# Kernel tuning notes

Hardware: AMD Instinct MI355X
Metric: run time of the kernel (lower is better)

## Reference

```python
import jax, jax.numpy as jnp
import numpy as np

NR_AST_NODES = 500_000
NR_CFG_NODES = 100_000
NR_MAPPED = 400_000
AST_DIM = 256
CFG_DIM = 256


def setup_inputs() -> dict:
    key = jax.random.key(0)
    k1, k2, k3, k4, k5 = jax.random.split(key, 5)
    prev = jax.random.normal(k1, (NR_AST_NODES, AST_DIM), dtype=jnp.float32)
    cfg = jax.random.normal(k2, (NR_CFG_NODES, CFG_DIM), dtype=jnp.float32)
    # key indices: unique (a subset permutation) so the scatter is well-defined,
    # mirroring the one-update-per-AST-node mapping in the original data.
    map_key = jax.random.permutation(k3, NR_AST_NODES)[:NR_MAPPED].astype(jnp.int32)
    map_val = jax.random.randint(k4, (NR_MAPPED,), 0, NR_CFG_NODES, dtype=jnp.int32)
    kw1, kw2 = jax.random.split(k5)
    W_update = jax.random.normal(kw1, (CFG_DIM, AST_DIM), dtype=jnp.float32) / np.sqrt(CFG_DIM)
    b_update = jnp.zeros((AST_DIM,), dtype=jnp.float32)
    W_gate = jax.random.normal(kw2, (AST_DIM + AST_DIM, AST_DIM), dtype=jnp.float32) / np.sqrt(2 * AST_DIM)
    b_gate = jnp.zeros((AST_DIM,), dtype=jnp.float32)
    return {
        "previous_ast_nodes_encodings": prev,
        "new_cfg_nodes_encodings": cfg,
        "map_key_indices": map_key,
        "map_val_indices": map_val,
        "W_update": W_update,
        "b_update": b_update,
        "W_gate": W_gate,
        "b_gate": b_gate,
    }


def reference(previous_ast_nodes_encodings, new_cfg_nodes_encodings,
              map_key_indices, map_val_indices,
              W_update, b_update, W_gate, b_gate):
    # gather: previous AST-node states and the macro (CFG) context per mapping entry
    prev_g = previous_ast_nodes_encodings[map_key_indices]        # [M, ast_dim]
    ctx_g = new_cfg_nodes_encodings[map_val_indices]              # [M, cfg_dim]
    # gated StateUpdater (GRU-like gate):
    #   u = tanh(ctx @ W_update + b_update)            -- projected state update
    #   z = sigmoid([prev; u] @ W_gate + b_gate)       -- update gate
    #   new = z * prev + (1 - z) * u
    u = jnp.tanh(ctx_g @ W_update + b_update)                      # [M, ast_dim]
    z = jax.nn.sigmoid(
        prev_g @ W_gate[:AST_DIM] + u @ W_gate[AST_DIM:] + b_gate)  # [M, ast_dim]
    new_states = z * prev_g + (1.0 - z) * u                        # [M, ast_dim]
    # scatter updated rows back into the dense AST-node encodings (dim 0)
    return previous_ast_nodes_encodings.at[map_key_indices].set(new_states)
```

## Files before the change

kernel.cpp:

```cpp
#include <hip/hip_runtime.h>
#include <hip/hip_bf16.h>

#define AST_DIM 256
#define NR_AST 500000
#define NR_CFG 100000
#define NR_MAP 400000
#define NBLK_MAIN ((NR_AST + 63) / 64)

typedef short short8 __attribute__((ext_vector_type(8)));
typedef float f32x4 __attribute__((ext_vector_type(4)));
typedef unsigned long long u64;
typedef unsigned int u32;

__device__ __forceinline__ unsigned short f2bf(float f) {
    u32 u = __float_as_uint(f);
    u += 0x7FFFu + ((u >> 16) & 1u);
    return (unsigned short)(u >> 16);
}
__device__ __forceinline__ float bf2f(unsigned short s) {
    return __uint_as_float(((u32)s) << 16);
}
__device__ __forceinline__ u64 pack4(f32x4 v) {
    __hip_bfloat162 lo = __float22bfloat162_rn(float2{v.x, v.y});
    __hip_bfloat162 hi = __float22bfloat162_rn(float2{v.z, v.w});
    return (u64)(*(u32*)&lo) | ((u64)(*(u32*)&hi) << 32);
}
__device__ __forceinline__ float fast_tanh(float x) {
    return 1.f - 2.f * __builtin_amdgcn_rcpf(__expf(2.f * x) + 1.f);
}
__device__ __forceinline__ float fast_sigmoid(float x) {
    return __builtin_amdgcn_rcpf(1.f + __expf(-x));
}
__device__ __forceinline__ void dma16(const void* g, void* l) {
    __builtin_amdgcn_global_load_lds((const __attribute__((address_space(1))) u32*)g,
                                     (__attribute__((address_space(3))) u32*)l, 16, 0, 0);
}

__global__ void convert_w(const float* __restrict__ Wu, const float* __restrict__ Wg,
                          unsigned short* __restrict__ wt) {
    int idx = blockIdx.x * 256 + threadIdx.x;
    if (idx >= 3 * 65536) return;
    int m = idx >> 16;
    int r = idx & 65535;
    int n = r >> 8;
    int k = r & 255;
    float v;
    if (m == 0)      v = Wu[k * 256 + n];
    else if (m == 1) v = Wg[k * 256 + n];
    else             v = Wg[(k + 256) * 256 + n];
    wt[idx] = f2bf(v);
}

__global__ void build_vor(const int* __restrict__ keys, const int* __restrict__ vals,
                          int* __restrict__ vor) {
    int i = blockIdx.x * 256 + threadIdx.x;
    if (i < NR_MAP) vor[keys[i]] = vals[i];
}

__global__ __launch_bounds__(512, 4) void compute_u(
    const float* __restrict__ cfg, const unsigned short* __restrict__ Wtu,
    const float* __restrict__ bu, unsigned short* __restrict__ u_all) {
    __shared__ __align__(16) unsigned char ctxb[64 * 512];

    const int tid = threadIdx.x;
    const int lane = tid & 63;
    const int wv = tid >> 6;
    const int ln15 = lane & 15;
    const int khi = lane >> 4;
    const int cb = wv * 32;
    const int m0 = blockIdx.x * 64;

    f32x4 v[8];
#pragma unroll
    for (int i = 0; i < 8; ++i) {
        int g = m0 + wv * 8 + i;
        if (g >= NR_CFG) g = NR_CFG - 1;
        v[i] = *((const f32x4*)(cfg + (size_t)g * AST_DIM) + lane);
    }
    __builtin_amdgcn_sched_barrier(0);
#pragma unroll
    for (int i = 0; i < 8; ++i) {
        int r = wv * 8 + i;
        int addr = (r << 9) + ((lane << 3) ^ ((r & 7) << 4));
        *(u64*)(ctxb + addr) = pack4(v[i]);
    }
    __syncthreads();

    const float b0 = bu[cb + ln15], b1 = bu[cb + 16 + ln15];
    f32x4 acc[4][2];
#pragma unroll
    for (int mt = 0; mt < 4; ++mt) {
        acc[mt][0] = f32x4{b0, b0, b0, b0};
        acc[mt][1] = f32x4{b1, b1, b1, b1};
    }
#pragma unroll
    for (int ks = 0; ks < 8; ++ks) {
        short8 a[4], b[2];
#pragma unroll
        for (int mt = 0; mt < 4; ++mt) {
            int row = mt * 16 + ln15;
            int addr = (row << 9) + (((ks << 6) + (khi << 4)) ^ ((row & 7) << 4));
            a[mt] = *(const short8*)(ctxb + addr);
        }
#pragma unroll
        for (int nt = 0; nt < 2; ++nt)
            b[nt] = *(const short8*)(Wtu + (cb + nt * 16 + ln15) * 256 + ks * 32 + khi * 8);
#pragma unroll
        for (int mt = 0; mt < 4; ++mt)
#pragma unroll
            for (int nt = 0; nt < 2; ++nt)
                acc[mt][nt] = __builtin_amdgcn_mfma_f32_16x16x32_bf16(a[mt], b[nt], acc[mt][nt], 0, 0, 0);
    }
#pragma unroll
    for (int mt = 0; mt < 4; ++mt)
#pragma unroll
        for (int rr = 0; rr < 4; ++rr) {
            int row = mt * 16 + khi * 4 + rr;
            int g = m0 + row;
            if (g < NR_CFG) {
#pragma unroll
                for (int nt = 0; nt < 2; ++nt) {
                    int col = cb + nt * 16 + ln15;
                    u_all[(size_t)g * AST_DIM + col] = f2bf(fast_tanh(acc[mt][nt][rr]));
                }
            }
        }
}

__global__ __launch_bounds__(512, 4) void stream_main(
    const float* __restrict__ prev, const unsigned short* __restrict__ u_all,
    const int* __restrict__ vor,
    const unsigned short* __restrict__ Wtgt, const unsigned short* __restrict__ Wtgb,
    const float* __restrict__ bg, float* __restrict__ out) {
    __shared__ __align__(16) unsigned char prvb[64 * 512];
    __shared__ __align__(16) unsigned char u_st[64 * 512];

    const int tid = threadIdx.x;
    const int lane = tid & 63;
    const int wv = tid >> 6;
    const int ln15 = lane & 15;
    const int khi = lane >> 4;
    const int ln31 = lane & 31;
    const int cb = wv * 32;
    const int m0 = blockIdx.x * 64;

    int vr = -1;
    if (m0 + lane < NR_AST) vr = vor[m0 + lane];

    f32x4 v[8];
#pragma unroll
    for (int i = 0; i < 8; ++i) {
        int g = m0 + wv * 8 + i;
        if (g >= NR_AST) g = NR_AST - 1;
        v[i] = *((const f32x4*)(prev + (size_t)g * AST_DIM) + lane);
    }
    __builtin_amdgcn_sched_barrier(0);
#pragma unroll
    for (int i = 0; i < 4; ++i) {
        int r0 = wv * 8 + i * 2;
        int row = r0 + (lane >> 5);
        int vidx = __shfl(vr, row);
        int vsrc = vidx < 0 ? 0 : vidx;
        const unsigned short* src = u_all + (size_t)vsrc * AST_DIM + ((ln31 ^ (row & 7)) << 3);
        dma16(src, u_st + (r0 << 9));
    }
    __builtin_amdgcn_sched_barrier(0);
#pragma unroll
    for (int i = 0; i < 8; ++i) {
        int r = wv * 8 + i;
        int g = m0 + r;
        int addr = (r << 9) + ((lane << 3) ^ ((r & 7) << 4));
        *(u64*)(prvb + addr) = pack4(v[i]);
        if (g < NR_AST && __shfl(vr, r) < 0)
            *((f32x4*)(out + (size_t)g * AST_DIM) + lane) = v[i];
    }
    __syncthreads();

    const float b0 = bg[cb + ln15], b1 = bg[cb + 16 + ln15];
    f32x4 acc[4][2];
#pragma unroll
    for (int mt = 0; mt < 4; ++mt) {
        acc[mt][0] = f32x4{b0, b0, b0, b0};
        acc[mt][1] = f32x4{b1, b1, b1, b1};
    }
#pragma unroll
    for (int ks = 0; ks < 8; ++ks) {
        short8 a[4], bfr[2];
#pragma unroll
        for (int mt = 0; mt < 4; ++mt) {
            int row = mt * 16 + ln15;
            int addr = (row << 9) + (((ks << 6) + (khi << 4)) ^ ((row & 7) << 4));
            a[mt] = *(const short8*)(prvb + addr);
        }
#pragma unroll
        for (int nt = 0; nt < 2; ++nt)
            bfr[nt] = *(const short8*)(Wtgt + (cb + nt * 16 + ln15) * 256 + ks * 32 + khi * 8);
#pragma unroll
        for (int mt = 0; mt < 4; ++mt)
#pragma unroll
            for (int nt = 0; nt < 2; ++nt)
                acc[mt][nt] = __builtin_amdgcn_mfma_f32_16x16x32_bf16(a[mt], bfr[nt], acc[mt][nt], 0, 0, 0);
    }
#pragma unroll
    for (int ks = 0; ks < 8; ++ks) {
        short8 a[4], bfr[2];
#pragma unroll
        for (int mt = 0; mt < 4; ++mt) {
            int row = mt * 16 + ln15;
            int addr = (row << 9) + ((((ks << 2) + khi) ^ (row & 7)) << 4);
            a[mt] = *(const short8*)(u_st + addr);
        }
#pragma unroll
        for (int nt = 0; nt < 2; ++nt)
            bfr[nt] = *(const short8*)(Wtgb + (cb + nt * 16 + ln15) * 256 + ks * 32 + khi * 8);
#pragma unroll
        for (int mt = 0; mt < 4; ++mt)
#pragma unroll
            for (int nt = 0; nt < 2; ++nt)
                acc[mt][nt] = __builtin_amdgcn_mfma_f32_16x16x32_bf16(a[mt], bfr[nt], acc[mt][nt], 0, 0, 0);
    }

#pragma unroll
    for (int mt = 0; mt < 4; ++mt)
#pragma unroll
        for (int rr = 0; rr < 4; ++rr) {
            int row = mt * 16 + khi * 4 + rr;
            int g = m0 + row;
            int vrow = __shfl(vr, row);
            if (g < NR_AST && vrow >= 0) {
                float* orow = out + (size_t)g * AST_DIM;
#pragma unroll
                for (int nt = 0; nt < 2; ++nt) {
                    int col = cb + nt * 16 + ln15;
                    float z = fast_sigmoid(acc[mt][nt][rr]);
                    float pf = bf2f(*(const unsigned short*)(prvb + (row << 9) + ((col << 1) ^ ((row & 7) << 4))));
                    float uv = bf2f(*(const unsigned short*)(u_st + (row << 9) +
                                    ((((col >> 3) ^ (row & 7)) << 4) + ((col & 7) << 1))));
                    orow[col] = fmaf(z, pf - uv, uv);
                }
            }
        }
}

__global__ void set_mask(const int* __restrict__ keys, unsigned char* __restrict__ mask) {
    int i = blockIdx.x * 256 + threadIdx.x;
    if (i < NR_MAP) mask[keys[i]] = 1;
}

__global__ void copy_unmapped(const float* __restrict__ prev,
                              const unsigned char* __restrict__ mask,
                              float* __restrict__ out) {
    const long long total = (long long)NR_AST * 64;
    for (long long i = (long long)blockIdx.x * blockDim.x + threadIdx.x; i < total;
         i += (long long)gridDim.x * blockDim.x) {
        int row = (int)(i >> 6);
        if (!mask[row])
            ((f32x4*)out)[i] = ((const f32x4*)prev)[i];
    }
}

__global__ __launch_bounds__(512, 4) void mixer_fused(
    const float* __restrict__ prev, const float* __restrict__ cfg,
    const int* __restrict__ keys, const int* __restrict__ vals,
    const unsigned short* __restrict__ Wtu, const unsigned short* __restrict__ Wtgt,
    const unsigned short* __restrict__ Wtgb, const float* __restrict__ bu,
    const float* __restrict__ bg, float* __restrict__ out) {
    __shared__ __align__(16) unsigned char ctx_lds[64 * 512];
    __shared__ __align__(16) unsigned char prv_lds[64 * 512];

    const int tid = threadIdx.x;
    const int lane = tid & 63;
    const int wave = tid >> 6;
    const int ln15 = lane & 15;
    const int khi = lane >> 4;
    const int cb = wave * 32;
    const int m0 = blockIdx.x * 64;

    const int kv = keys[m0 + lane];
    const int vv = vals[m0 + lane];

#pragma unroll 4
    for (int i = 0; i < 8; ++i) {
        int r = i * 8 + wave;
        f32x4 cv = *((const f32x4*)(cfg + (size_t)__shfl(vv, r) * AST_DIM) + lane);
        f32x4 pv = *((const f32x4*)(prev + (size_t)__shfl(kv, r) * AST_DIM) + lane);
        int addr = (r << 9) + ((lane << 3) ^ ((r & 7) << 4));
        *(u64*)(ctx_lds + addr) = pack4(cv);
        *(u64*)(prv_lds + addr) = pack4(pv);
    }
    __syncthreads();

    f32x4 acc[4][2];
    {
        float b0 = bu[cb + ln15], b1 = bu[cb + 16 + ln15];
        for (int mt = 0; mt < 4; ++mt) {
            acc[mt][0] = f32x4{b0, b0, b0, b0};
            acc[mt][1] = f32x4{b1, b1, b1, b1};
        }
    }
#pragma unroll
    for (int ks = 0; ks < 8; ++ks) {
        short8 a[4], b[2];
        for (int mt = 0; mt < 4; ++mt) {
            int row = mt * 16 + ln15;
            int addr = (row << 9) + (((ks << 6) + (khi << 4)) ^ ((row & 7) << 4));
            a[mt] = *(const short8*)(ctx_lds + addr);
        }
        for (int nt = 0; nt < 2; ++nt)
            b[nt] = *(const short8*)(Wtu + (cb + nt * 16 + ln15) * 256 + ks * 32 + khi * 8);
        for (int mt = 0; mt < 4; ++mt)
            for (int nt = 0; nt < 2; ++nt)
                acc[mt][nt] = __builtin_amdgcn_mfma_f32_16x16x32_bf16(a[mt], b[nt], acc[mt][nt], 0, 0, 0);
    }
    __syncthreads();
#pragma unroll
    for (int mt = 0; mt < 4; ++mt)
        for (int rr = 0; rr < 4; ++rr) {
            int row = mt * 16 + khi * 4 + rr;
            for (int nt = 0; nt < 2; ++nt) {
                int col = cb + nt * 16 + ln15;
                int addr = (row << 9) + ((col << 1) ^ ((row & 7) << 4));
                *(unsigned short*)(ctx_lds + addr) = f2bf(fast_tanh(acc[mt][nt][rr]));
            }
        }
    __syncthreads();
    {
        float b0 = bg[cb + ln15], b1 = bg[cb + 16 + ln15];
        for (int mt = 0; mt < 4; ++mt) {
            acc[mt][0] = f32x4{b0, b0, b0, b0};
            acc[mt][1] = f32x4{b1, b1, b1, b1};
        }
    }
#pragma unroll
    for (int ks = 0; ks < 8; ++ks) {
        short8 a[4], b[2];
        for (int mt = 0; mt < 4; ++mt) {
            int row = mt * 16 + ln15;
            int addr = (row << 9) + (((ks << 6) + (khi << 4)) ^ ((row & 7) << 4));
            a[mt] = *(const short8*)(prv_lds + addr);
        }
        for (int nt = 0; nt < 2; ++nt)
            b[nt] = *(const short8*)(Wtgt + (cb + nt * 16 + ln15) * 256 + ks * 32 + khi * 8);
        for (int mt = 0; mt < 4; ++mt)
            for (int nt = 0; nt < 2; ++nt)
                acc[mt][nt] = __builtin_amdgcn_mfma_f32_16x16x32_bf16(a[mt], b[nt], acc[mt][nt], 0, 0, 0);
    }
#pragma unroll
    for (int ks = 0; ks < 8; ++ks) {
        short8 a[4], b[2];
        for (int mt = 0; mt < 4; ++mt) {
            int row = mt * 16 + ln15;
            int addr = (row << 9) + (((ks << 6) + (khi << 4)) ^ ((row & 7) << 4));
            a[mt] = *(const short8*)(ctx_lds + addr);
        }
        for (int nt = 0; nt < 2; ++nt)
            b[nt] = *(const short8*)(Wtgb + (cb + nt * 16 + ln15) * 256 + ks * 32 + khi * 8);
        for (int mt = 0; mt < 4; ++mt)
            for (int nt = 0; nt < 2; ++nt)
                acc[mt][nt] = __builtin_amdgcn_mfma_f32_16x16x32_bf16(a[mt], b[nt], acc[mt][nt], 0, 0, 0);
    }
#pragma unroll
    for (int mt = 0; mt < 4; ++mt)
        for (int rr = 0; rr < 4; ++rr) {
            int row = mt * 16 + khi * 4 + rr;
            int key = __shfl(kv, row);
            float* orow = out + (size_t)key * AST_DIM;
            for (int nt = 0; nt < 2; ++nt) {
                int col = cb + nt * 16 + ln15;
                int ad = (row << 9) + ((col << 1) ^ ((row & 7) << 4));
                float z = fast_sigmoid(acc[mt][nt][rr]);
                float pf = bf2f(*(const unsigned short*)(prv_lds + ad));
                float uv = bf2f(*(const unsigned short*)(ctx_lds + ad));
                orow[col] = fmaf(z, pf - uv, uv);
            }
        }
}

extern "C" void kernel_launch(void* const* d_in, const int* in_sizes, int n_in,
                              void* d_out, int out_size, void* d_ws, size_t ws_size,
                              hipStream_t stream) {
    const float* prev = (const float*)d_in[0];
    const float* cfg = (const float*)d_in[1];
    const int* keys = (const int*)d_in[2];
    const int* vals = (const int*)d_in[3];
    const float* Wu = (const float*)d_in[4];
    const float* bu = (const float*)d_in[5];
    const float* Wg = (const float*)d_in[6];
    const float* bg = (const float*)d_in[7];
    float* out = (float*)d_out;

    unsigned short* wt = (unsigned short*)d_ws;
    int* vor = (int*)((char*)d_ws + (1u << 20));
    unsigned short* u_all = (unsigned short*)((char*)d_ws + (4u << 20));
    const size_t ws_needed = (size_t)(4u << 20) + (size_t)NR_CFG * AST_DIM * 2;

    convert_w<<<768, 256, 0, stream>>>(Wu, Wg, wt);
    if (ws_size >= ws_needed) {
        (void)hipMemsetAsync(vor, 0xFF, (size_t)NR_AST * 4, stream);
        build_vor<<<(NR_MAP + 255) / 256, 256, 0, stream>>>(keys, vals, vor);
        compute_u<<<(NR_CFG + 63) / 64, 512, 0, stream>>>(cfg, wt, bu, u_all);
        stream_main<<<NBLK_MAIN, 512, 0, stream>>>(prev, u_all, vor,
                                                   wt + 65536, wt + 2 * 65536, bg, out);
    } else {
        unsigned char* mask = (unsigned char*)d_ws + 3 * 65536 * 2;
        (void)hipMemsetAsync(mask, 0, NR_AST, stream);
        set_mask<<<(NR_MAP + 255) / 256, 256, 0, stream>>>(keys, mask);
        copy_unmapped<<<2048, 256, 0, stream>>>(prev, mask, out);
        mixer_fused<<<NR_MAP / 64, 512, 0, stream>>>(prev, cfg, keys, vals, wt, wt + 65536,
                                                     wt + 2 * 65536, bu, bg, out);
    }
}
```

Baseline: 448.9 us.

## Make stream_main persistent with software-pipelined prefetch of next tile

Turns the main streaming kernel into a persistent kernel with 512 blocks that loop over 64-row tiles. Each block issues the loads of the next tile's prev rows and vor indices before its MFMA compute on the current tile, waiting with a partial vmcnt so those loads overlap the math and the epilogue. This targets the launch and tail overhead of about 7.8k short blocks and aims to hide global-load latency. The cost is hand-tuned waitcnt counts that are fragile, extra barriers per tile, and less parallelism than the original grid if 512 blocks do not fill the machine.

```diff
diff --git a/kernel.cpp b/kernel.cpp
--- a/kernel.cpp
+++ b/kernel.cpp
@@ -5,7 +5,8 @@
 #define NR_AST 500000
 #define NR_CFG 100000
 #define NR_MAP 400000
-#define NBLK_MAIN ((NR_AST + 63) / 64)
+#define NT_TILES ((NR_AST + 63) / 64)
+#define NBLK 512
 
 typedef short short8 __attribute__((ext_vector_type(8)));
 typedef float f32x4 __attribute__((ext_vector_type(4)));
@@ -132,8 +133,8 @@
     const int* __restrict__ vor,
     const unsigned short* __restrict__ Wtgt, const unsigned short* __restrict__ Wtgb,
     const float* __restrict__ bg, float* __restrict__ out) {
-    __shared__ __align__(16) unsigned char prvb[64 * 512];
-    __shared__ __align__(16) unsigned char u_st[64 * 512];
+    __shared__ __align__(16) unsigned char P[64 * 512];
+    __shared__ __align__(16) unsigned char U[64 * 512];
 
     const int tid = threadIdx.x;
     const int lane = tid & 63;
@@ -142,11 +143,13 @@
     const int khi = lane >> 4;
     const int ln31 = lane & 31;
     const int cb = wv * 32;
-    const int m0 = blockIdx.x * 64;
-
-    int vr = -1;
-    if (m0 + lane < NR_AST) vr = vor[m0 + lane];
-
+
+    const float b0 = bg[cb + ln15], b1 = bg[cb + 16 + ln15];
+
+    int t = blockIdx.x;
+    int m0 = t * 64;
+    int vtmp = vor[m0 + lane < NR_AST ? m0 + lane : NR_AST - 1];
+    int vr = (m0 + lane < NR_AST) ? vtmp : -1;
     f32x4 v[8];
 #pragma unroll
     for (int i = 0; i < 8; ++i) {
@@ -154,92 +157,115 @@
         if (g >= NR_AST) g = NR_AST - 1;
         v[i] = *((const f32x4*)(prev + (size_t)g * AST_DIM) + lane);
     }
-    __builtin_amdgcn_sched_barrier(0);
-#pragma unroll
-    for (int i = 0; i < 4; ++i) {
-        int r0 = wv * 8 + i * 2;
-        int row = r0 + (lane >> 5);
-        int vidx = __shfl(vr, row);
-        int vsrc = vidx < 0 ? 0 : vidx;
-        const unsigned short* src = u_all + (size_t)vsrc * AST_DIM + ((ln31 ^ (row & 7)) << 3);
-        dma16(src, u_st + (r0 << 9));
-    }
-    __builtin_amdgcn_sched_barrier(0);
-#pragma unroll
-    for (int i = 0; i < 8; ++i) {
-        int r = wv * 8 + i;
-        int g = m0 + r;
-        int addr = (r << 9) + ((lane << 3) ^ ((r & 7) << 4));
-        *(u64*)(prvb + addr) = pack4(v[i]);
-        if (g < NR_AST && __shfl(vr, r) < 0)
-            *((f32x4*)(out + (size_t)g * AST_DIM) + lane) = v[i];
-    }
-    __syncthreads();
-
-    const float b0 = bg[cb + ln15], b1 = bg[cb + 16 + ln15];
-    f32x4 acc[4][2];
-#pragma unroll
-    for (int mt = 0; mt < 4; ++mt) {
-        acc[mt][0] = f32x4{b0, b0, b0, b0};
-        acc[mt][1] = f32x4{b1, b1, b1, b1};
-    }
-#pragma unroll
-    for (int ks = 0; ks < 8; ++ks) {
-        short8 a[4], bfr[2];
-#pragma unroll
-        for (int mt = 0; mt < 4; ++mt) {
-            int row = mt * 16 + ln15;
-            int addr = (row << 9) + (((ks << 6) + (khi << 4)) ^ ((row & 7) << 4));
-            a[mt] = *(const short8*)(prvb + addr);
-        }
-#pragma unroll
-        for (int nt = 0; nt < 2; ++nt)
-            bfr[nt] = *(const short8*)(Wtgt + (cb + nt * 16 + ln15) * 256 + ks * 32 + khi * 8);
+
+#pragma unroll 1
+    for (; t < NT_TILES; t += NBLK) {
+        m0 = t * 64;
+#pragma unroll
+        for (int i = 0; i < 8; ++i) {
+            int r = wv * 8 + i;
+            int g = m0 + r;
+            int addr = (r << 9) + ((lane << 3) ^ ((r & 7) << 4));
+            *(u64*)(P + addr) = pack4(v[i]);
+            if (g < NR_AST && __shfl(vr, r) < 0)
+                *((f32x4*)(out + (size_t)g * AST_DIM) + lane) = v[i];
+        }
+        __builtin_amdgcn_sched_barrier(0);
+#pragma unroll
+        for (int i = 0; i < 4; ++i) {
+            int r0 = wv * 8 + i * 2;
+            int row = r0 + (lane >> 5);
+            int vidx = __shfl(vr, row);
+            int vsrc = vidx < 0 ? 0 : vidx;
+            const unsigned short* src = u_all + (size_t)vsrc * AST_DIM + ((ln31 ^ (row & 7)) << 3);
+            dma16(src, U + (r0 << 9));
+        }
+        __builtin_amdgcn_sched_barrier(0);
+        int tn = t + NBLK;
+        if (tn >= NT_TILES) tn = NT_TILES - 1;
+        int mn = tn * 64;
+        int vtn = vor[mn + lane < NR_AST ? mn + lane : NR_AST - 1];
+        int vrn = (mn + lane < NR_AST) ? vtn : -1;
+#pragma unroll
+        for (int i = 0; i < 8; ++i) {
+            int g = mn + wv * 8 + i;
+            if (g >= NR_AST) g = NR_AST - 1;
+            v[i] = *((const f32x4*)(prev + (size_t)g * AST_DIM) + lane);
+        }
+        __builtin_amdgcn_sched_barrier(0);
+        asm volatile("s_waitcnt vmcnt(9) lgkmcnt(0)" ::: "memory");
+        __builtin_amdgcn_s_barrier();
+        __builtin_amdgcn_sched_barrier(0);
+
+        f32x4 acc[4][2];
+#pragma unroll
+        for (int mt = 0; mt < 4; ++mt) {
+            acc[mt][0] = f32x4{b0, b0, b0, b0};
+            acc[mt][1] = f32x4{b1, b1, b1, b1};
+        }
+#pragma unroll
+        for (int ks = 0; ks < 8; ++ks) {
+            short8 a[4], bfr[2];
+#pragma unroll
+            for (int mt = 0; mt < 4; ++mt) {
+                int row = mt * 16 + ln15;
+                int addr = (row << 9) + (((ks << 6) + (khi << 4)) ^ ((row & 7) << 4));
+                a[mt] = *(const short8*)(P + addr);
+            }
+#pragma unroll
+            for (int nt = 0; nt < 2; ++nt)
+                bfr[nt] = *(const short8*)(Wtgt + (cb + nt * 16 + ln15) * 256 + ks * 32 + khi * 8);
+#pragma unroll
+            for (int mt = 0; mt < 4; ++mt)
+#pragma unroll
+                for (int nt = 0; nt < 2; ++nt)
+                    acc[mt][nt] = __builtin_amdgcn_mfma_f32_16x16x32_bf16(a[mt], bfr[nt], acc[mt][nt], 0, 0, 0);
+        }
+#pragma unroll
+        for (int ks = 0; ks < 8; ++ks) {
+            short8 a[4], bfr[2];
+#pragma unroll
+            for (int mt = 0; mt < 4; ++mt) {
+                int row = mt * 16 + ln15;
+                int addr = (row << 9) + ((((ks << 2) + khi) ^ (row & 7)) << 4);
+                a[mt] = *(const short8*)(U + addr);
+            }
+#pragma unroll
+            for (int nt = 0; nt < 2; ++nt)
+                bfr[nt] = *(const short8*)(Wtgb + (cb + nt * 16 + ln15) * 256 + ks * 32 + khi * 8);
+#pragma unroll
+            for (int mt = 0; mt < 4; ++mt)
+#pragma unroll
+                for (int nt = 0; nt < 2; ++nt)
+                    acc[mt][nt] = __builtin_amdgcn_mfma_f32_16x16x32_bf16(a[mt], bfr[nt], acc[mt][nt], 0, 0, 0);
+        }
+
 #pragma unroll
         for (int mt = 0; mt < 4; ++mt)
 #pragma unroll
-            for (int nt = 0; nt < 2; ++nt)
-                acc[mt][nt] = __builtin_amdgcn_mfma_f32_16x16x32_bf16(a[mt], bfr[nt], acc[mt][nt], 0, 0, 0);
-    }
-#pragma unroll
-    for (int ks = 0; ks < 8; ++ks) {
-        short8 a[4], bfr[2];
-#pragma unroll
-        for (int mt = 0; mt < 4; ++mt) {
-            int row = mt * 16 + ln15;
-            int addr = (row << 9) + ((((ks << 2) + khi) ^ (row & 7)) << 4);
-            a[mt] = *(const short8*)(u_st + addr);
-        }
-#pragma unroll
-        for (int nt = 0; nt < 2; ++nt)
-            bfr[nt] = *(const short8*)(Wtgb + (cb + nt * 16 + ln15) * 256 + ks * 32 + khi * 8);
-#pragma unroll
-        for (int mt = 0; mt < 4; ++mt)
-#pragma unroll
-            for (int nt = 0; nt < 2; ++nt)
-                acc[mt][nt] = __builtin_amdgcn_mfma_f32_16x16x32_bf16(a[mt], bfr[nt], acc[mt][nt], 0, 0, 0);
-    }
-
-#pragma unroll
-    for (int mt = 0; mt < 4; ++mt)
-#pragma unroll
-        for (int rr = 0; rr < 4; ++rr) {
-            int row = mt * 16 + khi * 4 + rr;
-            int g = m0 + row;
-            int vrow = __shfl(vr, row);
-            if (g < NR_AST && vrow >= 0) {
-                float* orow = out + (size_t)g * AST_DIM;
-#pragma unroll
-                for (int nt = 0; nt < 2; ++nt) {
-                    int col = cb + nt * 16 + ln15;
-                    float z = fast_sigmoid(acc[mt][nt][rr]);
-                    float pf = bf2f(*(const unsigned short*)(prvb + (row << 9) + ((col << 1) ^ ((row & 7) << 4))));
-                    float uv = bf2f(*(const unsigned short*)(u_st + (row << 9) +
-                                    ((((col >> 3) ^ (row & 7)) << 4) + ((col & 7) << 1))));
-                    orow[col] = fmaf(z, pf - uv, uv);
+            for (int rr = 0; rr < 4; ++rr) {
+                int row = mt * 16 + khi * 4 + rr;
+                int g = m0 + row;
+                int vrow = __shfl(vr, row);
+                if (g < NR_AST && vrow >= 0) {
+                    float* orow = out + (size_t)g * AST_DIM;
+#pragma unroll
+                    for (int nt = 0; nt < 2; ++nt) {
+                        int col = cb + nt * 16 + ln15;
+                        float z = fast_sigmoid(acc[mt][nt][rr]);
+                        float pf = bf2f(*(const unsigned short*)(P + (row << 9) + ((col << 1) ^ ((row & 7) << 4))));
+                        float uv = bf2f(*(const unsigned short*)(U + (row << 9) +
+                                        ((((col >> 3) ^ (row & 7)) << 4) + ((col & 7) << 1))));
+                        orow[col] = fmaf(z, pf - uv, uv);
+                    }
                 }
             }
-        }
+        __builtin_amdgcn_sched_barrier(0);
+        asm volatile("s_waitcnt lgkmcnt(0)" ::: "memory");
+        __builtin_amdgcn_s_barrier();
+
+        vr = vrn;
+    }
 }
 
 __global__ void set_mask(const int* __restrict__ keys, unsigned char* __restrict__ mask) {
@@ -399,8 +425,8 @@
         (void)hipMemsetAsync(vor, 0xFF, (size_t)NR_AST * 4, stream);
         build_vor<<<(NR_MAP + 255) / 256, 256, 0, stream>>>(keys, vals, vor);
         compute_u<<<(NR_CFG + 63) / 64, 512, 0, stream>>>(cfg, wt, bu, u_all);
-        stream_main<<<NBLK_MAIN, 512, 0, stream>>>(prev, u_all, vor,
-                                                   wt + 65536, wt + 2 * 65536, bg, out);
+        stream_main<<<NBLK, 512, 0, stream>>>(prev, u_all, vor,
+                                              wt + 65536, wt + 2 * 65536, bg, out);
     } else {
         unsigned char* mask = (unsigned char*)d_ws + 3 * 65536 * 2;
         (void)hipMemsetAsync(mask, 0, NR_AST, stream);
```

After: 930.0 us. 2.07x slower.
